# Optimization experiments

Hardware: AMD Instinct MI355X
Metric: run time of the kernel (lower is better)

Reference implementation:

```python
import jax, jax.numpy as jnp
import numpy as np

B, S, H = 32, 256, 1024   # batch, seq_len, xlmr hidden
HL = 512                  # lstm hidden per direction
E = 256                   # entity_feature_size
L = 5                     # languages: en fr de es it
LN_EPS = 1e-5


def setup_inputs() -> dict:
    key = jax.random.key(0)
    ks = jax.random.split(key, 12)
    sc = 0.02
    sequence_output = jax.random.normal(ks[0], (B, S, H), jnp.float32)
    lengths = jax.random.randint(ks[1], (B,), S // 2, S + 1)
    attention_mask = (jnp.arange(S)[None, :] < lengths[:, None]).astype(jnp.int32)
    language_ids = jax.random.randint(ks[2], (B,), 0, L).astype(jnp.int64)
    # per-language adapter params (stacked over lang dim)
    W1 = jax.random.normal(ks[3], (L, H, H), jnp.float32) * sc
    b1 = jnp.zeros((L, H), jnp.float32)
    ln_g = jnp.ones((L, H), jnp.float32)
    ln_b = jnp.zeros((L, H), jnp.float32)
    W2 = jax.random.normal(ks[4], (L, H, H), jnp.float32) * sc
    b2 = jnp.zeros((L, H), jnp.float32)
    # BiLSTM params, torch gate order (i, f, g, o); b = b_ih + b_hh
    Wih_f = jax.random.normal(ks[5], (4 * HL, H), jnp.float32) * sc
    Whh_f = jax.random.normal(ks[6], (4 * HL, HL), jnp.float32) * sc
    b_f = jnp.zeros((4 * HL,), jnp.float32)
    Wih_b = jax.random.normal(ks[7], (4 * HL, H), jnp.float32) * sc
    Whh_b = jax.random.normal(ks[8], (4 * HL, HL), jnp.float32) * sc
    b_b = jnp.zeros((4 * HL,), jnp.float32)
    # projection 2*HL -> E
    Wp = jax.random.normal(ks[9], (E, 2 * HL), jnp.float32) * sc
    bp = jnp.zeros((E,), jnp.float32)
    return dict(sequence_output=sequence_output, attention_mask=attention_mask,
                language_ids=language_ids, W1=W1, b1=b1, ln_g=ln_g, ln_b=ln_b,
                W2=W2, b2=b2, Wih_f=Wih_f, Whh_f=Whh_f, b_f=b_f,
                Wih_b=Wih_b, Whh_b=Whh_b, b_b=b_b, Wp=Wp, bp=bp)


def _lstm_scan(x, mask, Wih, Whh, b):
    """x: [S,B,H], mask: [S,B,1] bool. Returns hidden states [S,B,HL].
    Masked steps keep state and emit 0 (pack/pad_packed semantics)."""
    h0 = jnp.zeros((x.shape[1], Whh.shape[1]), x.dtype)

    def step(carry, inp):
        h, c = carry
        x_t, m = inp
        gates = x_t @ Wih.T + h @ Whh.T + b
        i, f, g, o = jnp.split(gates, 4, axis=-1)
        c_new = jax.nn.sigmoid(f) * c + jax.nn.sigmoid(i) * jnp.tanh(g)
        h_new = jax.nn.sigmoid(o) * jnp.tanh(c_new)
        h = jnp.where(m, h_new, h)
        c = jnp.where(m, c_new, c)
        return (h, c), jnp.where(m, h_new, 0.0)

    _, ys = jax.lax.scan(step, (h0, h0), (x, mask))
    return ys


def reference(sequence_output, attention_mask, language_ids, W1, b1, ln_g, ln_b,
              W2, b2, Wih_f, Whh_f, b_f, Wih_b, Whh_b, b_b, Wp, bp):
    # --- all 5 language adapters on the full batch, then masked-sum ---
    h = jnp.einsum('bsh,lhd->lbsd', sequence_output, W1) + b1[:, None, None, :]
    mu = h.mean(-1, keepdims=True)
    var = h.var(-1, keepdims=True)
    h = (h - mu) * jax.lax.rsqrt(var + LN_EPS) * ln_g[:, None, None, :] + ln_b[:, None, None, :]
    h = jax.nn.relu(h)
    h = jnp.einsum('lbsd,ldh->lbsh', h, W2) + b2[:, None, None, :]
    onehot = jax.nn.one_hot(language_ids, L, dtype=h.dtype)          # [B,L]
    adapted = jnp.einsum('lbsh,bl->bsh', h, onehot)                  # [B,S,H]
    # --- BiLSTM over valid lengths (packed-sequence semantics) ---
    x = adapted.transpose(1, 0, 2)                                    # [S,B,H]
    m = attention_mask.astype(bool).T[:, :, None]                     # [S,B,1]
    ys_f = _lstm_scan(x, m, Wih_f, Whh_f, b_f)                        # [S,B,HL]
    ys_b = _lstm_scan(x[::-1], m[::-1], Wih_b, Whh_b, b_b)[::-1]      # [S,B,HL]
    lstm_out = jnp.concatenate([ys_f, ys_b], -1).transpose(1, 0, 2)   # [B,S,2HL]
    return lstm_out @ Wp.T + bp                                       # [B,S,E]
```

## Files before the change

### kernel.cpp

```cpp
#include <hip/hip_runtime.h>

typedef __bf16 bft;
typedef bft bf16x8 __attribute__((ext_vector_type(8)));
typedef bft bf16x4 __attribute__((ext_vector_type(4)));
typedef bft bf16x2 __attribute__((ext_vector_type(2)));
typedef float f32x4 __attribute__((ext_vector_type(4)));
typedef unsigned long long u64;
typedef unsigned int u32;
typedef u32 u32x4 __attribute__((ext_vector_type(4)));

#define LN_EPS 1e-5f


__device__ __forceinline__ float sigmoidf_(float x) {
    return 1.f / (1.f + __expf(-x));
}
__device__ __forceinline__ float tanhf_(float x) {
    float e = __expf(-2.f * fabsf(x));
    float t = (1.f - e) / (1.f + e);
    return copysignf(t, x);
}

__global__ void cvt_f32_bf16(const float* __restrict__ in, bft* __restrict__ out, int n4) {
    int i = blockIdx.x * blockDim.x + threadIdx.x;
    if (i < n4) {
        float4 v = ((const float4*)in)[i];
        bf16x4 o = { (bft)v.x, (bft)v.y, (bft)v.z, (bft)v.w };
        ((bf16x4*)out)[i] = o;
    }
}

__global__ void zero_u32(u32* __restrict__ p, int n) {
    int i = blockIdx.x * blockDim.x + threadIdx.x;
    if (i < n) p[i] = 0u;
}

__global__ __launch_bounds__(256) void transpose_cvt_w(
    const float* __restrict__ W1, const float* __restrict__ W2,
    bft* __restrict__ W1t, bft* __restrict__ W2t)
{
    __shared__ float tile[32][33];
    int z = blockIdx.z;
    int l = z >> 1;
    const float* src = ((z & 1) ? W2 : W1) + ((size_t)l << 20);
    bft* dst = ((z & 1) ? W2t : W1t) + ((size_t)l << 20);
    int tx = threadIdx.x & 31, ty = threadIdx.x >> 5;
    int bx = blockIdx.x * 32, by = blockIdx.y * 32;
    for (int r = ty; r < 32; r += 8)
        tile[r][tx] = src[(size_t)(by + r) * 1024 + bx + tx];
    __syncthreads();
    for (int r = ty; r < 32; r += 8)
        dst[(size_t)(bx + r) * 1024 + by + tx] = (bft)tile[tx][r];
}

__global__ __launch_bounds__(256) void gemm_bt(
    const bft* __restrict__ A, const bft* __restrict__ Bt,
    const float* __restrict__ bias, const int* __restrict__ langs,
    int langStrideB, int langStrideBias,
    float* __restrict__ outF, bft* __restrict__ outB,
    int remapLog, int remapMul, int ldc)
{
    const int K = 1024;
    int tn = blockIdx.x, tm = blockIdx.y;
    int row0 = tm * 128, col0 = tn * 128;
    int lang = langs ? langs[row0 >> 8] : 0;
    const bft* Ap = A + (size_t)row0 * K;
    const bft* Bp = Bt + (size_t)lang * langStrideB + (size_t)col0 * K;
    const float* biasp = bias + (size_t)lang * langStrideBias + col0;

    __shared__ bft As[128 * 32];
    __shared__ bft Bs[128 * 32];

    int t = threadIdx.x;
    int lane = t & 63, wave = t >> 6;
    int wm = wave & 1, wn = wave >> 1;
    int lrow = lane & 15, quad = lane >> 4;

    f32x4 acc[4][4] = {};

    for (int k0 = 0; k0 < K; k0 += 32) {
        __syncthreads();
        for (int c = t; c < 512; c += 256) {
            int r = c >> 2, co = (c & 3) << 3;
            *(uint4*)(As + r * 32 + co) = *(const uint4*)(Ap + (size_t)r * K + k0 + co);
            *(uint4*)(Bs + r * 32 + co) = *(const uint4*)(Bp + (size_t)r * K + k0 + co);
        }
        __syncthreads();
        bf16x8 af[4], bfr[4];
#pragma unroll
        for (int i = 0; i < 4; ++i)
            af[i] = *(const bf16x8*)(As + (wm * 64 + i * 16 + lrow) * 32 + quad * 8);
#pragma unroll
        for (int j = 0; j < 4; ++j)
            bfr[j] = *(const bf16x8*)(Bs + (wn * 64 + j * 16 + lrow) * 32 + quad * 8);
#pragma unroll
        for (int i = 0; i < 4; ++i)
#pragma unroll
            for (int j = 0; j < 4; ++j)
                acc[i][j] = __builtin_amdgcn_mfma_f32_16x16x32_bf16(af[i], bfr[j], acc[i][j], 0, 0, 0);
    }

#pragma unroll
    for (int i = 0; i < 4; ++i) {
#pragma unroll
        for (int j = 0; j < 4; ++j) {
#pragma unroll
            for (int r = 0; r < 4; ++r) {
                int m = wm * 64 + i * 16 + quad * 4 + r;
                int n = wn * 64 + j * 16 + lrow;
                int grow = row0 + m;
                int orow = remapLog ? ((grow & ((1 << remapLog) - 1)) * remapMul + (grow >> remapLog))
                                    : grow;
                float v = acc[i][j][r] + biasp[n];
                size_t idx = (size_t)orow * ldc + col0 + n;
                if (outF) outF[idx] = v;
                else outB[idx] = (bft)v;
            }
        }
    }
}

__global__ __launch_bounds__(256) void ln_relu_kernel(
    const float* __restrict__ h1, bft* __restrict__ a2,
    const float* __restrict__ ln_g, const float* __restrict__ ln_b,
    const int* __restrict__ langs)
{
    int row = blockIdx.x;
    int lang = langs[row >> 8];
    const float* x = h1 + (size_t)row * 1024;
    int t = threadIdx.x;
    float4 v = ((const float4*)x)[t];
    float s = v.x + v.y + v.z + v.w;
    float ss = v.x * v.x + v.y * v.y + v.z * v.z + v.w * v.w;
#pragma unroll
    for (int off = 32; off > 0; off >>= 1) {
        s += __shfl_down(s, off, 64);
        ss += __shfl_down(ss, off, 64);
    }
    __shared__ float red[8];
    int wave = t >> 6, lane = t & 63;
    if (lane == 0) { red[wave] = s; red[4 + wave] = ss; }
    __syncthreads();
    float S = red[0] + red[1] + red[2] + red[3];
    float SS = red[4] + red[5] + red[6] + red[7];
    float mean = S * (1.f / 1024.f);
    float var = SS * (1.f / 1024.f) - mean * mean;
    float inv = rsqrtf(var + LN_EPS);
    float4 g = ((const float4*)(ln_g + (size_t)lang * 1024))[t];
    float4 b = ((const float4*)(ln_b + (size_t)lang * 1024))[t];
    float y0 = fmaxf(0.f, (v.x - mean) * inv * g.x + b.x);
    float y1 = fmaxf(0.f, (v.y - mean) * inv * g.y + b.y);
    float y2 = fmaxf(0.f, (v.z - mean) * inv * g.z + b.z);
    float y3 = fmaxf(0.f, (v.w - mean) * inv * g.w + b.w);
    bf16x4 o = { (bft)y0, (bft)y1, (bft)y2, (bft)y3 };
    ((bf16x4*)(a2 + (size_t)row * 1024))[t] = o;
}

__global__ __launch_bounds__(256) void bilstm_kernel(
    const bft* __restrict__ gin_f, const bft* __restrict__ gin_b,
    const bft* __restrict__ Whh_f, const bft* __restrict__ Whh_b,
    const int* __restrict__ mask, bft* __restrict__ ys,
    u32* __restrict__ hg, u32* __restrict__ ctr)
{
    __shared__ u64 smem[8192];
    bft* Wlds = (bft*)smem;
    bft* hs   = (bft*)(smem + 4096);
    u32* hsd  = (u32*)(smem + 4096);
    float* gatesF = (float*)(smem + 4096);

    int blk = blockIdx.x;
    int dir = blk >> 6;
    int gslice = blk & 63;
    int jbase = gslice << 3;
    const bft* Whh = dir ? Whh_b : Whh_f;
    const bft* gin = dir ? gin_b : gin_f;

    int t = threadIdx.x;
    int lane = t & 63, wave = t >> 6;
    int wm = wave & 1, wn = wave >> 1;
    int lrow = lane & 15, quad = lane >> 4;
    int am = t >> 2, jp = t & 3;

    for (int i = 0; i < 8; ++i) {
        int c = t + i * 256;
        int r = c >> 6, b64 = c & 63;
        int gate = r >> 3, jj = r & 7;
        int phys = b64 ^ (r & 7);
        ((uint4*)Wlds)[r * 64 + phys] =
            ((const uint4*)(Whh + (size_t)(gate * 512 + jbase + jj) * 512))[b64];
    }

    float cs0 = 0.f, cs1 = 0.f, hp0 = 0.f, hp1 = 0.f;
    u32* ysU = (u32*)ys;
    int mloS = t >> 6;
    int b16S = t & 63;

    for (int it = 0; it < 256; ++it) {
        int tt = dir ? (255 - it) : it;

        bf16x2 gpre[4];
        int mk = 0;
        if (t < 128) {
            size_t gb = ((size_t)tt * 32 + am) * 1024 + (jbase >> 1) + jp;
#pragma unroll
            for (int g = 0; g < 4; ++g)
                gpre[g] = ((const bf16x2*)gin)[gb + g * 256];
            mk = mask[am * 256 + tt];
        }

        if (it == 0) {
#pragma unroll
            for (int i = 0; i < 16; ++i)
                smem[4096 + t + i * 256] = 0ull;
        } else {
            if (wave == 0) {
                const u32* cp = ctr + (size_t)(dir * 256 + it) * 128 + (lane < 8 ? lane * 16 : 0);
                for (;;) {
                    u32 c = 8u;
                    if (lane < 8)
                        c = __hip_atomic_load(cp, __ATOMIC_RELAXED, __HIP_MEMORY_SCOPE_AGENT);
                    if (__all(c >= 8u)) break;
                    __builtin_amdgcn_s_sleep(2);
                }
            }
            __syncthreads();
            const u32* hq = hg + (size_t)(dir * 2 + (it & 1)) * 8192;
            u32x4 r[8];
#pragma unroll
            for (int i = 0; i < 8; ++i)
                asm volatile("global_load_dwordx4 %0, %1, off sc0 sc1"
                             : "=v"(r[i]) : "v"(hq + i * 1024 + t * 4) : "memory");
            asm volatile("s_waitcnt vmcnt(0)" ::: "memory");
#pragma unroll
            for (int i = 0; i < 8; ++i) {
                int m = i * 4 + mloS;
                *(u32x4*)(hsd + m * 256 + ((b16S ^ (m & 7)) << 2)) = r[i];
            }
        }
        __syncthreads();

        f32x4 acc0 = {}, acc1 = {};
        int arow = wm * 16 + lrow, brow = wn * 16 + lrow;
#pragma unroll
        for (int kk = 0; kk < 16; ++kk) {
            int b16 = kk * 4 + quad;
            bf16x8 a = *(const bf16x8*)(hs   + arow * 512 + ((b16 ^ (arow & 7)) << 3));
            bf16x8 b = *(const bf16x8*)(Wlds + brow * 512 + ((b16 ^ (brow & 7)) << 3));
            if (kk & 1) acc1 = __builtin_amdgcn_mfma_f32_16x16x32_bf16(a, b, acc1, 0, 0, 0);
            else        acc0 = __builtin_amdgcn_mfma_f32_16x16x32_bf16(a, b, acc0, 0, 0, 0);
        }
        f32x4 acc = acc0 + acc1;
        __syncthreads();

#pragma unroll
        for (int r = 0; r < 4; ++r)
            gatesF[(wm * 16 + quad * 4 + r) * 33 + wn * 16 + lrow] = acc[r];
        __syncthreads();

        u32 ypack = 0;
        if (t < 128) {
            int l0 = 2 * jp;
            const float* gr = gatesF + am * 33;
            float xi0 = gr[l0]      + (float)gpre[0][0], xi1 = gr[l0 + 1]      + (float)gpre[0][1];
            float xf0 = gr[8 + l0]  + (float)gpre[1][0], xf1 = gr[8 + l0 + 1]  + (float)gpre[1][1];
            float xg0 = gr[16 + l0] + (float)gpre[2][0], xg1 = gr[16 + l0 + 1] + (float)gpre[2][1];
            float xo0 = gr[24 + l0] + (float)gpre[3][0], xo1 = gr[24 + l0 + 1] + (float)gpre[3][1];
            float cn0 = sigmoidf_(xf0) * cs0 + sigmoidf_(xi0) * tanhf_(xg0);
            float cn1 = sigmoidf_(xf1) * cs1 + sigmoidf_(xi1) * tanhf_(xg1);
            float hn0 = sigmoidf_(xo0) * tanhf_(cn0);
            float hn1 = sigmoidf_(xo1) * tanhf_(cn1);
            union { bf16x2 v; u32 u; } hpk, ypk;
            if (mk) {
                cs0 = cn0; cs1 = cn1; hp0 = hn0; hp1 = hn1;
                hpk.v = bf16x2{ (bft)hn0, (bft)hn1 };
                ypk.u = hpk.u;
            } else {
                hpk.v = bf16x2{ (bft)hp0, (bft)hp1 };
                ypk.u = 0u;
            }
            ypack = ypk.u;
            u32* ha = hg + (size_t)(dir * 2 + ((it + 1) & 1)) * 8192 + am * 256 + gslice * 4 + jp;
            u32 hv = hpk.u;
            asm volatile("global_store_dword %0, %1, off sc0 sc1" :: "v"(ha), "v"(hv) : "memory");
        }
        asm volatile("s_waitcnt vmcnt(0)" ::: "memory");
        __syncthreads();
        if (t == 0 && it < 255)
            __hip_atomic_fetch_add(ctr + (size_t)(dir * 256 + it + 1) * 128 + (gslice & 7) * 16,
                                   1u, __ATOMIC_RELAXED, __HIP_MEMORY_SCOPE_AGENT);
        if (t < 128)
            ysU[((size_t)tt * 32 + am) * 512 + dir * 256 + gslice * 4 + jp] = ypack;
    }
}

extern "C" void kernel_launch(void* const* d_in, const int* in_sizes, int n_in,
                              void* d_out, int out_size, void* d_ws, size_t ws_size,
                              hipStream_t stream)
{
    const float* X     = (const float*)d_in[0];
    const int*   amask = (const int*)d_in[1];
    const int*   langs = (const int*)d_in[2];
    const float* W1    = (const float*)d_in[3];
    const float* b1    = (const float*)d_in[4];
    const float* ln_g  = (const float*)d_in[5];
    const float* ln_b  = (const float*)d_in[6];
    const float* W2    = (const float*)d_in[7];
    const float* b2    = (const float*)d_in[8];
    const float* Wih_f = (const float*)d_in[9];
    const float* Whh_f = (const float*)d_in[10];
    const float* b_f   = (const float*)d_in[11];
    const float* Wih_b = (const float*)d_in[12];
    const float* Whh_b = (const float*)d_in[13];
    const float* b_b   = (const float*)d_in[14];
    const float* Wp    = (const float*)d_in[15];
    const float* bp    = (const float*)d_in[16];
    float* out = (float*)d_out;

    char* ws = (char*)d_ws;
    size_t off = 0;
    auto alloc = [&](size_t bytes) -> void* {
        void* p = ws + off;
        off += (bytes + 255) & ~(size_t)255;
        return p;
    };
    bft* Xbf   = (bft*)alloc(8192ull * 1024 * 2);
    bft* W1t   = (bft*)alloc(5ull * 1024 * 1024 * 2);
    bft* W2t   = (bft*)alloc(5ull * 1024 * 1024 * 2);
    bft* Wihf  = (bft*)alloc(2048ull * 1024 * 2);
    bft* Wihb  = (bft*)alloc(2048ull * 1024 * 2);
    bft* Whhf  = (bft*)alloc(2048ull * 512 * 2);
    bft* Whhb  = (bft*)alloc(2048ull * 512 * 2);
    bft* Wpb   = (bft*)alloc(256ull * 1024 * 2);
    float* h1  = (float*)alloc(8192ull * 1024 * 4);
    bft* a2    = (bft*)alloc(8192ull * 1024 * 2);
    bft* adapt = (bft*)alloc(8192ull * 1024 * 2);
    bft* ginf  = (bft*)alloc(256ull * 32 * 2048 * 2);
    bft* ginb  = (bft*)alloc(256ull * 32 * 2048 * 2);
    bft* ysb   = (bft*)alloc(256ull * 32 * 1024 * 2);
    u32* hg    = (u32*)alloc(2ull * 2 * 32 * 256 * 4);
    u32* ctr   = (u32*)alloc(2ull * 256 * 8 * 16 * 4);
    (void)ws_size; (void)in_sizes; (void)n_in; (void)out_size;

    auto cvt = [&](const float* src, bft* dst, int n) {
        int n4 = n >> 2;
        hipLaunchKernelGGL(cvt_f32_bf16, dim3((n4 + 255) / 256), dim3(256), 0, stream, src, dst, n4);
    };
    cvt(X, Xbf, 8192 * 1024);
    cvt(Wih_f, Wihf, 2048 * 1024);
    cvt(Wih_b, Wihb, 2048 * 1024);
    cvt(Whh_f, Whhf, 2048 * 512);
    cvt(Whh_b, Whhb, 2048 * 512);
    cvt(Wp, Wpb, 256 * 1024);
    hipLaunchKernelGGL(zero_u32, dim3(256), dim3(256), 0, stream, ctr, 65536);
    hipLaunchKernelGGL(transpose_cvt_w, dim3(32, 32, 10), dim3(256), 0, stream, W1, W2, W1t, W2t);

    hipLaunchKernelGGL(gemm_bt, dim3(8, 64), dim3(256), 0, stream,
        Xbf, W1t, b1, langs, 1024 * 1024, 1024, h1, (bft*)nullptr, 0, 0, 1024);
    hipLaunchKernelGGL(ln_relu_kernel, dim3(8192), dim3(256), 0, stream, h1, a2, ln_g, ln_b, langs);
    hipLaunchKernelGGL(gemm_bt, dim3(8, 64), dim3(256), 0, stream,
        a2, W2t, b2, langs, 1024 * 1024, 1024, (float*)nullptr, adapt, 0, 0, 1024);
    hipLaunchKernelGGL(gemm_bt, dim3(16, 64), dim3(256), 0, stream,
        adapt, Wihf, b_f, (const int*)nullptr, 0, 0, (float*)nullptr, ginf, 8, 32, 2048);
    hipLaunchKernelGGL(gemm_bt, dim3(16, 64), dim3(256), 0, stream,
        adapt, Wihb, b_b, (const int*)nullptr, 0, 0, (float*)nullptr, ginb, 8, 32, 2048);
    {
        void* args[] = { (void*)&ginf, (void*)&ginb, (void*)&Whhf, (void*)&Whhb,
                         (void*)&amask, (void*)&ysb, (void*)&hg, (void*)&ctr };
        hipLaunchCooperativeKernel((const void*)bilstm_kernel, dim3(128), dim3(256), args, 0, stream);
    }
    hipLaunchKernelGGL(gemm_bt, dim3(2, 64), dim3(256), 0, stream,
        ysb, Wpb, bp, (const int*)nullptr, 0, 0, out, (bft*)nullptr, 5, 256, 256);
}
```

Baseline: 1.236 ms.

## Keep LSTM recurrent weights in registers and interleave gate layout

Permutes the input-projection weights and bias so each hidden unit's four gates are adjacent. Each lane can then finish the LSTM cell update directly from its MFMA accumulator, with no LDS gate round-trip and two fewer barriers per step. The recurrent weight slice is held in registers as MFMA operands instead of in LDS, which shrinks shared memory. Cross-block synchronisation moves from per-step atomic counters to per-block monotonic flags. The costs are higher register pressure and extra permutation kernels in the preprocessing stage.

```diff
diff --git a/kernel.cpp b/kernel.cpp
--- a/kernel.cpp
+++ b/kernel.cpp
@@ -33,6 +33,22 @@
 __global__ void zero_u32(u32* __restrict__ p, int n) {
     int i = blockIdx.x * blockDim.x + threadIdx.x;
     if (i < n) p[i] = 0u;
+}
+
+__global__ __launch_bounds__(256) void cvt_permute_wih(
+    const float* __restrict__ in, bft* __restrict__ out)
+{
+    int r = blockIdx.x;
+    int src = (r & 3) * 512 + (r >> 2);
+    int t = threadIdx.x;
+    float4 v = ((const float4*)(in + (size_t)src * 1024))[t];
+    bf16x4 o = { (bft)v.x, (bft)v.y, (bft)v.z, (bft)v.w };
+    ((bf16x4*)(out + (size_t)r * 1024))[t] = o;
+}
+
+__global__ void permute_bias(const float* __restrict__ in, float* __restrict__ out) {
+    int t = blockIdx.x * blockDim.x + threadIdx.x;
+    if (t < 2048) out[t] = in[(t & 3) * 512 + (t >> 2)];
 }
 
 __global__ __launch_bounds__(256) void transpose_cvt_w(
@@ -160,13 +176,11 @@
     const bft* __restrict__ gin_f, const bft* __restrict__ gin_b,
     const bft* __restrict__ Whh_f, const bft* __restrict__ Whh_b,
     const int* __restrict__ mask, bft* __restrict__ ys,
-    u32* __restrict__ hg, u32* __restrict__ ctr)
-{
-    __shared__ u64 smem[8192];
-    bft* Wlds = (bft*)smem;
-    bft* hs   = (bft*)(smem + 4096);
-    u32* hsd  = (u32*)(smem + 4096);
-    float* gatesF = (float*)(smem + 4096);
+    u32* __restrict__ hg, u32* __restrict__ flg)
+{
+    __shared__ u64 smem[4096];
+    bft* hs  = (bft*)smem;
+    u32* hsd = (u32*)smem;
 
     int blk = blockIdx.x;
     int dir = blk >> 6;
@@ -179,48 +193,43 @@
     int lane = t & 63, wave = t >> 6;
     int wm = wave & 1, wn = wave >> 1;
     int lrow = lane & 15, quad = lane >> 4;
-    int am = t >> 2, jp = t & 3;
-
-    for (int i = 0; i < 8; ++i) {
-        int c = t + i * 256;
-        int r = c >> 6, b64 = c & 63;
-        int gate = r >> 3, jj = r & 7;
-        int phys = b64 ^ (r & 7);
-        ((uint4*)Wlds)[r * 64 + phys] =
-            ((const uint4*)(Whh + (size_t)(gate * 512 + jbase + jj) * 512))[b64];
-    }
-
-    float cs0 = 0.f, cs1 = 0.f, hp0 = 0.f, hp1 = 0.f;
+
+    bf16x8 wf[16];
+    {
+        int row32 = wm * 16 + lrow;
+        int jl = row32 >> 2, g = row32 & 3;
+        const bft* wp = Whh + (size_t)(g * 512 + jbase + jl) * 512 + quad * 8;
+#pragma unroll
+        for (int kk = 0; kk < 16; ++kk)
+            wf[kk] = *(const bf16x8*)(wp + kk * 32);
+    }
+
+    int batch = wn * 16 + lrow;
+    int jl_out = wm * 4 + quad;
+    const int* mrow = mask + batch * 256;
     u32* ysU = (u32*)ys;
-    int mloS = t >> 6;
-    int b16S = t & 63;
+    int mloS = t >> 6, b16S = t & 63;
+
+    float cs = 0.f, hp = 0.f;
 
     for (int it = 0; it < 256; ++it) {
         int tt = dir ? (255 - it) : it;
 
-        bf16x2 gpre[4];
-        int mk = 0;
-        if (t < 128) {
-            size_t gb = ((size_t)tt * 32 + am) * 1024 + (jbase >> 1) + jp;
-#pragma unroll
-            for (int g = 0; g < 4; ++g)
-                gpre[g] = ((const bf16x2*)gin)[gb + g * 256];
-            mk = mask[am * 256 + tt];
-        }
+        bf16x4 gv = *(const bf16x4*)(gin + ((size_t)(tt * 32 + batch) * 2048
+                                            + (size_t)(jbase + jl_out) * 4));
+        int mk = mrow[tt];
 
         if (it == 0) {
 #pragma unroll
             for (int i = 0; i < 16; ++i)
-                smem[4096 + t + i * 256] = 0ull;
+                smem[t + i * 256] = 0ull;
         } else {
             if (wave == 0) {
-                const u32* cp = ctr + (size_t)(dir * 256 + it) * 128 + (lane < 8 ? lane * 16 : 0);
+                const u32* fp = flg + dir * 64 + lane;
                 for (;;) {
-                    u32 c = 8u;
-                    if (lane < 8)
-                        c = __hip_atomic_load(cp, __ATOMIC_RELAXED, __HIP_MEMORY_SCOPE_AGENT);
-                    if (__all(c >= 8u)) break;
-                    __builtin_amdgcn_s_sleep(2);
+                    u32 f = __hip_atomic_load(fp, __ATOMIC_RELAXED, __HIP_MEMORY_SCOPE_AGENT);
+                    if (__all(f >= (u32)it)) break;
+                    __builtin_amdgcn_s_sleep(1);
                 }
             }
             __syncthreads();
@@ -240,56 +249,41 @@
         __syncthreads();
 
         f32x4 acc0 = {}, acc1 = {};
-        int arow = wm * 16 + lrow, brow = wn * 16 + lrow;
 #pragma unroll
         for (int kk = 0; kk < 16; ++kk) {
             int b16 = kk * 4 + quad;
-            bf16x8 a = *(const bf16x8*)(hs   + arow * 512 + ((b16 ^ (arow & 7)) << 3));
-            bf16x8 b = *(const bf16x8*)(Wlds + brow * 512 + ((b16 ^ (brow & 7)) << 3));
-            if (kk & 1) acc1 = __builtin_amdgcn_mfma_f32_16x16x32_bf16(a, b, acc1, 0, 0, 0);
-            else        acc0 = __builtin_amdgcn_mfma_f32_16x16x32_bf16(a, b, acc0, 0, 0, 0);
+            bf16x8 b = *(const bf16x8*)(hs + batch * 512 + ((b16 ^ (batch & 7)) << 3));
+            if (kk & 1) acc1 = __builtin_amdgcn_mfma_f32_16x16x32_bf16(wf[kk], b, acc1, 0, 0, 0);
+            else        acc0 = __builtin_amdgcn_mfma_f32_16x16x32_bf16(wf[kk], b, acc0, 0, 0, 0);
         }
         f32x4 acc = acc0 + acc1;
-        __syncthreads();
-
-#pragma unroll
-        for (int r = 0; r < 4; ++r)
-            gatesF[(wm * 16 + quad * 4 + r) * 33 + wn * 16 + lrow] = acc[r];
-        __syncthreads();
-
-        u32 ypack = 0;
-        if (t < 128) {
-            int l0 = 2 * jp;
-            const float* gr = gatesF + am * 33;
-            float xi0 = gr[l0]      + (float)gpre[0][0], xi1 = gr[l0 + 1]      + (float)gpre[0][1];
-            float xf0 = gr[8 + l0]  + (float)gpre[1][0], xf1 = gr[8 + l0 + 1]  + (float)gpre[1][1];
-            float xg0 = gr[16 + l0] + (float)gpre[2][0], xg1 = gr[16 + l0 + 1] + (float)gpre[2][1];
-            float xo0 = gr[24 + l0] + (float)gpre[3][0], xo1 = gr[24 + l0 + 1] + (float)gpre[3][1];
-            float cn0 = sigmoidf_(xf0) * cs0 + sigmoidf_(xi0) * tanhf_(xg0);
-            float cn1 = sigmoidf_(xf1) * cs1 + sigmoidf_(xi1) * tanhf_(xg1);
-            float hn0 = sigmoidf_(xo0) * tanhf_(cn0);
-            float hn1 = sigmoidf_(xo1) * tanhf_(cn1);
-            union { bf16x2 v; u32 u; } hpk, ypk;
-            if (mk) {
-                cs0 = cn0; cs1 = cn1; hp0 = hn0; hp1 = hn1;
-                hpk.v = bf16x2{ (bft)hn0, (bft)hn1 };
-                ypk.u = hpk.u;
-            } else {
-                hpk.v = bf16x2{ (bft)hp0, (bft)hp1 };
-                ypk.u = 0u;
-            }
-            ypack = ypk.u;
-            u32* ha = hg + (size_t)(dir * 2 + ((it + 1) & 1)) * 8192 + am * 256 + gslice * 4 + jp;
-            u32 hv = hpk.u;
-            asm volatile("global_store_dword %0, %1, off sc0 sc1" :: "v"(ha), "v"(hv) : "memory");
+
+        float xi = acc[0] + (float)gv[0];
+        float xf = acc[1] + (float)gv[1];
+        float xg = acc[2] + (float)gv[2];
+        float xo = acc[3] + (float)gv[3];
+        float cn = sigmoidf_(xf) * cs + sigmoidf_(xi) * tanhf_(xg);
+        float hn = sigmoidf_(xo) * tanhf_(cn);
+        if (mk) { cs = cn; hp = hn; }
+        union { bft h; unsigned short u; } hc; hc.h = (bft)hp;
+        u32 own = (u32)hc.u | ((mk ? (u32)hc.u : 0u) << 16);
+        u32 par = __shfl_xor(own, 16, 64);
+        u32 hpair = (own & 0xffffu) | (par << 16);
+        u32 ypair = (own >> 16) | (par & 0xffff0000u);
+
+        if (!(lane & 16)) {
+            u32* ha = hg + (size_t)(dir * 2 + ((it + 1) & 1)) * 8192
+                         + batch * 256 + (jbase >> 1) + wm * 2 + (quad >> 1);
+            asm volatile("global_store_dword %0, %1, off sc0 sc1" :: "v"(ha), "v"(hpair) : "memory");
         }
         asm volatile("s_waitcnt vmcnt(0)" ::: "memory");
         __syncthreads();
         if (t == 0 && it < 255)
-            __hip_atomic_fetch_add(ctr + (size_t)(dir * 256 + it + 1) * 128 + (gslice & 7) * 16,
-                                   1u, __ATOMIC_RELAXED, __HIP_MEMORY_SCOPE_AGENT);
-        if (t < 128)
-            ysU[((size_t)tt * 32 + am) * 512 + dir * 256 + gslice * 4 + jp] = ypack;
+            __hip_atomic_store(flg + dir * 64 + gslice, (u32)(it + 1),
+                               __ATOMIC_RELAXED, __HIP_MEMORY_SCOPE_AGENT);
+        if (!(lane & 16))
+            ysU[((size_t)tt * 32 + batch) * 512 + dir * 256
+                + (jbase >> 1) + wm * 2 + (quad >> 1)] = ypair;
     }
 }
 
@@ -337,8 +331,10 @@
     bft* ginf  = (bft*)alloc(256ull * 32 * 2048 * 2);
     bft* ginb  = (bft*)alloc(256ull * 32 * 2048 * 2);
     bft* ysb   = (bft*)alloc(256ull * 32 * 1024 * 2);
+    float* pbf = (float*)alloc(2048ull * 4);
+    float* pbb = (float*)alloc(2048ull * 4);
     u32* hg    = (u32*)alloc(2ull * 2 * 32 * 256 * 4);
-    u32* ctr   = (u32*)alloc(2ull * 256 * 8 * 16 * 4);
+    u32* flg   = (u32*)alloc(2ull * 64 * 4);
     (void)ws_size; (void)in_sizes; (void)n_in; (void)out_size;
 
     auto cvt = [&](const float* src, bft* dst, int n) {
@@ -346,12 +342,14 @@
         hipLaunchKernelGGL(cvt_f32_bf16, dim3((n4 + 255) / 256), dim3(256), 0, stream, src, dst, n4);
     };
     cvt(X, Xbf, 8192 * 1024);
-    cvt(Wih_f, Wihf, 2048 * 1024);
-    cvt(Wih_b, Wihb, 2048 * 1024);
+    hipLaunchKernelGGL(cvt_permute_wih, dim3(2048), dim3(256), 0, stream, Wih_f, Wihf);
+    hipLaunchKernelGGL(cvt_permute_wih, dim3(2048), dim3(256), 0, stream, Wih_b, Wihb);
     cvt(Whh_f, Whhf, 2048 * 512);
     cvt(Whh_b, Whhb, 2048 * 512);
     cvt(Wp, Wpb, 256 * 1024);
-    hipLaunchKernelGGL(zero_u32, dim3(256), dim3(256), 0, stream, ctr, 65536);
+    hipLaunchKernelGGL(permute_bias, dim3(8), dim3(256), 0, stream, b_f, pbf);
+    hipLaunchKernelGGL(permute_bias, dim3(8), dim3(256), 0, stream, b_b, pbb);
+    hipLaunchKernelGGL(zero_u32, dim3(1), dim3(256), 0, stream, flg, 128);
     hipLaunchKernelGGL(transpose_cvt_w, dim3(32, 32, 10), dim3(256), 0, stream, W1, W2, W1t, W2t);
 
     hipLaunchKernelGGL(gemm_bt, dim3(8, 64), dim3(256), 0, stream,
@@ -360,12 +358,12 @@
     hipLaunchKernelGGL(gemm_bt, dim3(8, 64), dim3(256), 0, stream,
         a2, W2t, b2, langs, 1024 * 1024, 1024, (float*)nullptr, adapt, 0, 0, 1024);
     hipLaunchKernelGGL(gemm_bt, dim3(16, 64), dim3(256), 0, stream,
-        adapt, Wihf, b_f, (const int*)nullptr, 0, 0, (float*)nullptr, ginf, 8, 32, 2048);
+        adapt, Wihf, pbf, (const int*)nullptr, 0, 0, (float*)nullptr, ginf, 8, 32, 2048);
     hipLaunchKernelGGL(gemm_bt, dim3(16, 64), dim3(256), 0, stream,
-        adapt, Wihb, b_b, (const int*)nullptr, 0, 0, (float*)nullptr, ginb, 8, 32, 2048);
+        adapt, Wihb, pbb, (const int*)nullptr, 0, 0, (float*)nullptr, ginb, 8, 32, 2048);
     {
         void* args[] = { (void*)&ginf, (void*)&ginb, (void*)&Whhf, (void*)&Whhb,
-                         (void*)&amask, (void*)&ysb, (void*)&hg, (void*)&ctr };
+                         (void*)&amask, (void*)&ysb, (void*)&hg, (void*)&flg };
         hipLaunchCooperativeKernel((const void*)bilstm_kernel, dim3(128), dim3(256), args, 0, stream);
     }
     hipLaunchKernelGGL(gemm_bt, dim3(2, 64), dim3(256), 0, stream,
```

Measured after the change: 1.326 ms. 7.3% more time.
